# Optimization experiments

Hardware: AMD Instinct MI355X
Metric: run time of the kernel (lower is better)

Reference implementation:

```python
import jax, jax.numpy as jnp
import numpy as np
from jax import lax

SHIFT_SIZE = 5
PAD = SHIFT_SIZE // 2


def _shift(xn, axis):
    """xn: (B, C, Hp, Wp, Dp) zero-padded volume. Split channels into
    SHIFT_SIZE chunks and roll each chunk by shift in [-PAD, PAD] along `axis`."""
    chunks = jnp.split(xn, SHIFT_SIZE, axis=1)
    shifted = [jnp.roll(c, s, axis=axis) for c, s in zip(chunks, range(-PAD, PAD + 1))]
    return jnp.concatenate(shifted, axis=1)


def _shift_tokens(x, H, W, D, axis):
    """x: (B, N, C) tokens -> shifted tokens (B, N, C). axis=2 shifts H, axis=3 shifts W."""
    B, N, C = x.shape
    xn = x.transpose(0, 2, 1).reshape(B, C, H, W, D)
    xn = jnp.pad(xn, ((0, 0), (0, 0), (PAD, PAD), (PAD, PAD), (PAD, PAD)))
    xs = _shift(xn, axis)
    xs = xs[:, :, PAD:PAD + H, PAD:PAD + W, PAD:PAD + D]
    return xs.reshape(B, C, N).transpose(0, 2, 1)


def setup_inputs() -> dict:
    key = jax.random.key(0)
    ks = jax.random.split(key, 4)
    B, H, W, D = 2, 32, 32, 32
    N = H * W * D
    Cin, Ch = 160, 640
    return {
        "x": jax.random.normal(ks[0], (B, N, Cin), jnp.float32),
        "fc1_w": jax.random.normal(ks[1], (Ch, Cin), jnp.float32) * 0.02,
        "fc1_b": jnp.zeros((Ch,), jnp.float32),
        "dw_w": jax.random.normal(ks[2], (Ch, 1, 3, 3, 3), jnp.float32) * (2.0 / 27.0) ** 0.5,
        "dw_b": jnp.zeros((Ch,), jnp.float32),
        "fc2_w": jax.random.normal(ks[3], (Cin, Ch), jnp.float32) * 0.02,
        "fc2_b": jnp.zeros((Cin,), jnp.float32),
        "H": H, "W": W, "D": D,
    }


def reference(x, fc1_w, fc1_b, dw_w, dw_b, fc2_w, fc2_b, H, W, D):
    B, N, Cin = x.shape
    Ch = fc1_w.shape[0]
    # shift block 1: roll along H (axis 2)
    xs = _shift_tokens(x, H, W, D, axis=2)
    # fc1
    h = jnp.einsum('bnc,hc->bnh', xs, fc1_w) + fc1_b  # (B, N, Ch)
    # depthwise 3x3x3 conv
    hv = h.transpose(0, 2, 1).reshape(B, Ch, H, W, D)
    hv = lax.conv_general_dilated(
        hv, dw_w, window_strides=(1, 1, 1), padding='SAME',
        feature_group_count=Ch,
        dimension_numbers=('NCDHW', 'OIDHW', 'NCDHW'))
    hv = hv + dw_b[None, :, None, None, None]
    hv = jax.nn.gelu(hv, approximate=False)
    h = hv.reshape(B, Ch, N).transpose(0, 2, 1)
    # shift block 2: roll along W (axis 3)
    hs = _shift_tokens(h, H, W, D, axis=3)
    # fc2
    out = jnp.einsum('bnh,oh->bno', hs, fc2_w) + fc2_b  # (B, N, Cin)
    return out
```

## Files before the change

### kernel.cpp

```cpp
#include <hip/hip_runtime.h>
#include <hip/hip_bf16.h>
#include <math.h>

#define DEVI __device__ __forceinline__

typedef __bf16 bf16;
typedef _Float16 f16;
typedef bf16 bf16x4 __attribute__((ext_vector_type(4)));
typedef bf16 bf16x8 __attribute__((ext_vector_type(8)));
typedef f16 f16x8 __attribute__((ext_vector_type(8)));
typedef float f32x4 __attribute__((ext_vector_type(4)));

constexpr int Bb = 2, Hh = 32, Ww = 32, Dd = 32;
constexpr int Nn = Hh * Ww * Dd;
constexpr int BN = Bb * Nn;
constexpr int CIN = 160, CHH = 640;

constexpr size_t XB_OFF = 0;
constexpr size_t W1_OFF = XB_OFF + (size_t)BN * CIN * 2;
constexpr size_t W2_OFF = W1_OFF + (size_t)CHH * CIN * 2;
constexpr size_t WTH_OFF = W2_OFF + (size_t)CIN * CHH * 2;
constexpr size_t ZP_OFF = WTH_OFF + 34816;
constexpr size_t H1_OFF = ZP_OFF + 8192;
constexpr size_t H2_OFF = H1_OFF + (size_t)BN * CHH * 2;

DEVI void async16(const void* g, void* l) {
  __builtin_amdgcn_global_load_lds(
      (const __attribute__((address_space(1))) void*)g,
      (__attribute__((address_space(3))) void*)l, 16, 0, 0);
}

__global__ __launch_bounds__(256) void k_prep_x(const float* __restrict__ x,
                                                bf16* __restrict__ xb, int n4) {
  int i = blockIdx.x * 256 + threadIdx.x;
  if (i >= n4) return;
  float4 v = reinterpret_cast<const float4*>(x)[i];
  bf16x4 o;
  o[0] = (bf16)v.x; o[1] = (bf16)v.y; o[2] = (bf16)v.z; o[3] = (bf16)v.w;
  reinterpret_cast<bf16x4*>(xb)[i] = o;
}

__global__ __launch_bounds__(256) void k_prep_w(const float* __restrict__ fc1w,
                                                const float* __restrict__ fc2w,
                                                const float* __restrict__ dww,
                                                bf16* __restrict__ w1b,
                                                bf16* __restrict__ w2b,
                                                f16* __restrict__ wTh,
                                                unsigned* __restrict__ zp) {
  int i = blockIdx.x * 256 + threadIdx.x;
  const int NW = CHH * CIN;
  if (i < NW) {
    w1b[i] = (bf16)fc1w[i];
  } else if (i < 2 * NW) {
    int j = i - NW;
    w2b[j] = (bf16)fc2w[j];
  } else if (i < 2 * NW + 27 * CHH) {
    int j = i - 2 * NW;
    int ch = j / 27, tap = j % 27;
    wTh[tap * CHH + ch] = (f16)dww[j];
  } else if (i < 2 * NW + 27 * CHH + 2048) {
    zp[i - (2 * NW + 27 * CHH)] = 0u;
  }
}

__global__ __launch_bounds__(256) void k_gemm1(const bf16* __restrict__ xb,
                                               const bf16* __restrict__ w1b,
                                               const float* __restrict__ fc1b,
                                               const bf16* __restrict__ zp,
                                               f16* __restrict__ h1h) {
  __shared__ bf16 lsA[128 * 32];
  __shared__ bf16 lsB[128 * 32];
  const int tid = threadIdx.x;
  const int lane = tid & 63, wave = tid >> 6;
  const int row0 = blockIdx.x * 128;
  const int col0 = blockIdx.y * 128;

  f32x4 acc[4][4] = {};
  const int wr = wave >> 1, wc = wave & 1;
  const int rl = lane & 15, kb = (lane >> 4) * 8;

  for (int ks = 0; ks < 5; ++ks) {
    __syncthreads();
    const int s = ks - 2;
#pragma unroll
    for (int issue = 0; issue < 2; ++issue) {
      int c = issue * 256 + tid;
      int ar = c >> 2;
      int kc = (c & 3) * 8;
      int t = row0 + ar;
      int h = (t >> 10) & 31;
      int hs = h - s;
      const bf16* src;
      if (hs >= 0 && hs < 32)
        src = xb + (size_t)(t - s * 1024) * CIN + ks * 32 + kc;
      else
        src = zp + (size_t)(c & 63) * 8;
      async16(src, (char*)lsA + issue * 4096 + wave * 1024);
    }
#pragma unroll
    for (int issue = 0; issue < 2; ++issue) {
      int c = issue * 256 + tid;
      int br = c >> 2;
      int kc = (c & 3) * 8;
      const bf16* src = w1b + (size_t)(col0 + br) * CIN + ks * 32 + kc;
      async16(src, (char*)lsB + issue * 4096 + wave * 1024);
    }
    __syncthreads();
    bf16x8 af[4], bfr[4];
#pragma unroll
    for (int mi = 0; mi < 4; ++mi)
      af[mi] = *(const bf16x8*)&lsA[(wr * 64 + mi * 16 + rl) * 32 + kb];
#pragma unroll
    for (int ni = 0; ni < 4; ++ni)
      bfr[ni] = *(const bf16x8*)&lsB[(wc * 64 + ni * 16 + rl) * 32 + kb];
#pragma unroll
    for (int mi = 0; mi < 4; ++mi)
#pragma unroll
      for (int ni = 0; ni < 4; ++ni)
        acc[mi][ni] = __builtin_amdgcn_mfma_f32_16x16x32_bf16(af[mi], bfr[ni], acc[mi][ni], 0, 0, 0);
  }
  const int rq = lane >> 4;
#pragma unroll
  for (int mi = 0; mi < 4; ++mi) {
#pragma unroll
    for (int ni = 0; ni < 4; ++ni) {
      int col = col0 + wc * 64 + ni * 16 + rl;
      float bias = fc1b[col];
#pragma unroll
      for (int r = 0; r < 4; ++r) {
        int row = row0 + wr * 64 + mi * 16 + rq * 4 + r;
        h1h[(size_t)row * CHH + col] = (f16)(acc[mi][ni][r] + bias);
      }
    }
  }
}

__global__ __launch_bounds__(256) void k_conv(const f16* __restrict__ h1h,
                                              const f16* __restrict__ wTh,
                                              const float* __restrict__ dwb,
                                              const bf16* __restrict__ zp,
                                              bf16* __restrict__ h2b) {
  __shared__ f16 lw[27 * 64];
  __shared__ float lb[64];
  const int tid = threadIdx.x;
  const int cg = blockIdx.y;
#pragma unroll
  for (int i = 0; i < 7; ++i) {
    int idx = i * 256 + tid;
    if (idx < 27 * 64) lw[idx] = wTh[(idx >> 6) * CHH + cg * 64 + (idx & 63)];
  }
  if (tid < 64) lb[tid] = dwb[cg * 64 + tid];
  __syncthreads();

  const int lane = tid & 63, wave = tid >> 6;
  const int line = blockIdx.x * 4 + wave;
  const int c8 = lane & 7, dq = lane >> 3;
  const int d0 = dq * 4;
  const int ch0 = cg * 64 + c8 * 8;
  const int w = line & 31, h = (line >> 5) & 31;
  const f16* zpf = (const f16*)zp;

  f16x8 acc[4];
  {
    f16x8 binit;
#pragma unroll
    for (int j = 0; j < 8; ++j) binit[j] = (f16)lb[c8 * 8 + j];
    acc[0] = binit; acc[1] = binit; acc[2] = binit; acc[3] = binit;
  }

  const ptrdiff_t base_line = (ptrdiff_t)line * 32 * CHH + ch0;

#pragma unroll
  for (int kz = 0; kz < 3; ++kz) {
    int hz = h + kz - 1;
    if ((unsigned)hz >= 32u) continue;
#pragma unroll
    for (int ky = 0; ky < 3; ++ky) {
      int wy = w + ky - 1;
      if ((unsigned)wy >= 32u) continue;
      const f16* rowbase = h1h + base_line +
                           (ptrdiff_t)((kz - 1) * 1024 + (ky - 1) * 32) * CHH;
      f16x8 wt[3];
#pragma unroll
      for (int kx = 0; kx < 3; ++kx)
        wt[kx] = *(const f16x8*)&lw[((kz * 9 + ky * 3 + kx) << 6) + c8 * 8];
      f16x8 v[6];
#pragma unroll
      for (int j = 0; j < 6; ++j) {
        int td = d0 - 1 + j;
        const f16* p = ((unsigned)td < 32u) ? rowbase + (ptrdiff_t)td * CHH
                                            : zpf + c8 * 8;
        v[j] = *(const f16x8*)p;
      }
#pragma unroll
      for (int o = 0; o < 4; ++o)
#pragma unroll
        for (int kx = 0; kx < 3; ++kx)
          acc[o] = v[o + kx] * wt[kx] + acc[o];
    }
  }

#pragma unroll
  for (int o = 0; o < 4; ++o) {
    bf16x8 ovec;
#pragma unroll
    for (int j = 0; j < 8; ++j) {
      float xv = (float)acc[o][j];
      float zt = 0.7978845608f * xv + 0.03567740814f * (xv * xv * xv);
      zt = fminf(fmaxf(zt, -15.0f), 15.0f);
      float e = __builtin_exp2f(zt * 2.8853900817779268f);
      float tnh = (e - 1.0f) / (e + 1.0f);
      ovec[j] = (bf16)(0.5f * xv * (1.0f + tnh));
    }
    *(bf16x8*)&h2b[base_line + (ptrdiff_t)(d0 + o) * CHH] = ovec;
  }
}

__global__ __launch_bounds__(256) void k_gemm2(const bf16* __restrict__ h2b,
                                               const bf16* __restrict__ w2b,
                                               const float* __restrict__ fc2b,
                                               const bf16* __restrict__ zp,
                                               float* __restrict__ out) {
  __shared__ bf16 lsA[128 * 64];
  __shared__ bf16 lsB[160 * 64];
  const int tid = threadIdx.x, lane = tid & 63, wave = tid >> 6;
  const int row0 = blockIdx.x * 128;
  const int rl = lane & 15, kb = (lane >> 4) * 8;

  f32x4 acc[2][10] = {};

  for (int kt = 0; kt < 10; ++kt) {
    __syncthreads();
    const int k0 = kt * 64;
    const int s = (k0 >> 7) - 2;
#pragma unroll
    for (int issue = 0; issue < 4; ++issue) {
      int c = issue * 256 + tid;
      int ar = c >> 3;
      int kc = (c & 7) * 8;
      int t = row0 + ar;
      int w = (t >> 5) & 31;
      int wsv = w - s;
      const bf16* src;
      if (wsv >= 0 && wsv < 32)
        src = h2b + (size_t)(t - s * 32) * CHH + k0 + kc;
      else
        src = zp + (size_t)(c & 63) * 8;
      async16(src, (char*)lsA + issue * 4096 + wave * 1024);
    }
#pragma unroll
    for (int issue = 0; issue < 5; ++issue) {
      int c = issue * 256 + tid;
      int br = c >> 3;
      int kc = (c & 7) * 8;
      const bf16* src = w2b + (size_t)br * CHH + k0 + kc;
      async16(src, (char*)lsB + issue * 4096 + wave * 1024);
    }
    __syncthreads();
#pragma unroll
    for (int kk = 0; kk < 2; ++kk) {
      bf16x8 af[2], bfr[10];
#pragma unroll
      for (int mi = 0; mi < 2; ++mi)
        af[mi] = *(const bf16x8*)&lsA[(wave * 32 + mi * 16 + rl) * 64 + kk * 32 + kb];
#pragma unroll
      for (int ni = 0; ni < 10; ++ni)
        bfr[ni] = *(const bf16x8*)&lsB[(ni * 16 + rl) * 64 + kk * 32 + kb];
#pragma unroll
      for (int mi = 0; mi < 2; ++mi)
#pragma unroll
        for (int ni = 0; ni < 10; ++ni)
          acc[mi][ni] = __builtin_amdgcn_mfma_f32_16x16x32_bf16(af[mi], bfr[ni], acc[mi][ni], 0, 0, 0);
    }
  }
  const int rq = lane >> 4;
#pragma unroll
  for (int mi = 0; mi < 2; ++mi) {
#pragma unroll
    for (int ni = 0; ni < 10; ++ni) {
      int col = ni * 16 + rl;
      float bias = fc2b[col];
#pragma unroll
      for (int r = 0; r < 4; ++r) {
        int row = row0 + wave * 32 + mi * 16 + rq * 4 + r;
        out[(size_t)row * CIN + col] = acc[mi][ni][r] + bias;
      }
    }
  }
}

extern "C" void kernel_launch(void* const* d_in, const int* in_sizes, int n_in,
                              void* d_out, int out_size, void* d_ws, size_t ws_size,
                              hipStream_t stream) {
  const float* x    = (const float*)d_in[0];
  const float* fc1w = (const float*)d_in[1];
  const float* fc1b = (const float*)d_in[2];
  const float* dww  = (const float*)d_in[3];
  const float* dwb  = (const float*)d_in[4];
  const float* fc2w = (const float*)d_in[5];
  const float* fc2b = (const float*)d_in[6];

  char* ws = (char*)d_ws;
  bf16* xb   = (bf16*)(ws + XB_OFF);
  bf16* w1b  = (bf16*)(ws + W1_OFF);
  bf16* w2b  = (bf16*)(ws + W2_OFF);
  f16*  wTh  = (f16*)(ws + WTH_OFF);
  bf16* zp   = (bf16*)(ws + ZP_OFF);
  f16*  h1h  = (f16*)(ws + H1_OFF);
  bf16* h2b  = (bf16*)(ws + H2_OFF);
  float* out = (float*)d_out;

  k_prep_x<<<(BN * CIN / 4) / 256, 256, 0, stream>>>(x, xb, BN * CIN / 4);
  k_prep_w<<<943, 256, 0, stream>>>(fc1w, fc2w, dww, w1b, w2b, wTh, (unsigned*)zp);
  dim3 g1(512, 5);
  k_gemm1<<<g1, 256, 0, stream>>>(xb, w1b, fc1b, zp, h1h);
  dim3 gc(BN / 32 / 4, 10);
  k_conv<<<gc, 256, 0, stream>>>(h1h, wTh, dwb, zp, h2b);
  k_gemm2<<<512, 256, 0, stream>>>(h2b, w2b, fc2b, zp, out);
}
```

Measured before the change: 146.6 us.

## Store fc1 output into zero-padded volume to remove conv boundary checks

gemm1 now writes its output into a 34x34x34 zero-padded halo layout. A new kernel zeroes only the halo cells, so the depthwise conv loads all 27 taps without branching or selecting a zero-page pointer. The xb and h2b buffers now share one workspace region, and the GELU tanh form is rewritten as a sigmoid using exp2 and a hardware reciprocal. This adds an extra zeroing launch and a larger h1 buffer, and the sigmoid rewrite drops the clamp, so it relies on the reciprocal's behaviour at very large inputs.

```diff
diff --git a/kernel.cpp b/kernel.cpp
--- a/kernel.cpp
+++ b/kernel.cpp
@@ -15,14 +15,15 @@
 constexpr int Nn = Hh * Ww * Dd;
 constexpr int BN = Bb * Nn;
 constexpr int CIN = 160, CHH = 640;
-
-constexpr size_t XB_OFF = 0;
-constexpr size_t W1_OFF = XB_OFF + (size_t)BN * CIN * 2;
-constexpr size_t W2_OFF = W1_OFF + (size_t)CHH * CIN * 2;
+constexpr int PD = 34;
+constexpr int PT = PD * PD * PD;
+
+constexpr size_t W1_OFF  = 0;
+constexpr size_t W2_OFF  = W1_OFF + (size_t)CHH * CIN * 2;
 constexpr size_t WTH_OFF = W2_OFF + (size_t)CIN * CHH * 2;
-constexpr size_t ZP_OFF = WTH_OFF + 34816;
-constexpr size_t H1_OFF = ZP_OFF + 8192;
-constexpr size_t H2_OFF = H1_OFF + (size_t)BN * CHH * 2;
+constexpr size_t ZP_OFF  = WTH_OFF + 34816;
+constexpr size_t U_OFF   = 458752;
+constexpr size_t H1P_OFF = U_OFF + (size_t)BN * CHH * 2;
 
 DEVI void async16(const void* g, void* l) {
   __builtin_amdgcn_global_load_lds(
@@ -63,11 +64,27 @@
   }
 }
 
+__global__ __launch_bounds__(256) void k_zero_pad(f16* __restrict__ h1p) {
+  int g = blockIdx.x * 256 + threadIdx.x;
+  int p = g / 80;
+  int c = g - p * 80;
+  if (p >= 2 * PT) return;
+  int r = p % PT;
+  int hp = r / (PD * PD);
+  int r2 = r % (PD * PD);
+  int wp = r2 / PD, dp = r2 % PD;
+  bool pad = (hp == 0) | (hp == PD - 1) | (wp == 0) | (wp == PD - 1) |
+             (dp == 0) | (dp == PD - 1);
+  if (!pad) return;
+  f16x8 z = {};
+  *(f16x8*)&h1p[(size_t)p * CHH + c * 8] = z;
+}
+
 __global__ __launch_bounds__(256) void k_gemm1(const bf16* __restrict__ xb,
                                                const bf16* __restrict__ w1b,
                                                const float* __restrict__ fc1b,
                                                const bf16* __restrict__ zp,
-                                               f16* __restrict__ h1h) {
+                                               f16* __restrict__ h1p) {
   __shared__ bf16 lsA[128 * 32];
   __shared__ bf16 lsB[128 * 32];
   const int tid = threadIdx.x;
@@ -122,23 +139,26 @@
   const int rq = lane >> 4;
 #pragma unroll
   for (int mi = 0; mi < 4; ++mi) {
+    int rowq = row0 + wr * 64 + mi * 16 + rq * 4;
+    int bq = rowq >> 15;
+    int nq = rowq & 32767;
+    int hq = nq >> 10, wq = (nq >> 5) & 31, dq = nq & 31;
+    size_t pos = (size_t)((bq * PD + hq + 1) * PD + (wq + 1)) * PD + (dq + 1);
+    f16* dst0 = h1p + pos * CHH;
 #pragma unroll
     for (int ni = 0; ni < 4; ++ni) {
       int col = col0 + wc * 64 + ni * 16 + rl;
       float bias = fc1b[col];
 #pragma unroll
-      for (int r = 0; r < 4; ++r) {
-        int row = row0 + wr * 64 + mi * 16 + rq * 4 + r;
-        h1h[(size_t)row * CHH + col] = (f16)(acc[mi][ni][r] + bias);
-      }
-    }
-  }
-}
-
-__global__ __launch_bounds__(256) void k_conv(const f16* __restrict__ h1h,
+      for (int r = 0; r < 4; ++r)
+        dst0[(size_t)r * CHH + col] = (f16)(acc[mi][ni][r] + bias);
+    }
+  }
+}
+
+__global__ __launch_bounds__(256) void k_conv(const f16* __restrict__ h1p,
                                               const f16* __restrict__ wTh,
                                               const float* __restrict__ dwb,
-                                              const bf16* __restrict__ zp,
                                               bf16* __restrict__ h2b) {
   __shared__ f16 lw[27 * 64];
   __shared__ float lb[64];
@@ -157,8 +177,10 @@
   const int c8 = lane & 7, dq = lane >> 3;
   const int d0 = dq * 4;
   const int ch0 = cg * 64 + c8 * 8;
-  const int w = line & 31, h = (line >> 5) & 31;
-  const f16* zpf = (const f16*)zp;
+  const int w = line & 31, h = (line >> 5) & 31, b = line >> 10;
+
+  const size_t cidx = (size_t)((b * PD + h) * PD + w) * PD + d0;
+  const f16* base = h1p + cidx * CHH + ch0;
 
   f16x8 acc[4];
   {
@@ -168,30 +190,19 @@
     acc[0] = binit; acc[1] = binit; acc[2] = binit; acc[3] = binit;
   }
 
-  const ptrdiff_t base_line = (ptrdiff_t)line * 32 * CHH + ch0;
-
 #pragma unroll
   for (int kz = 0; kz < 3; ++kz) {
-    int hz = h + kz - 1;
-    if ((unsigned)hz >= 32u) continue;
 #pragma unroll
     for (int ky = 0; ky < 3; ++ky) {
-      int wy = w + ky - 1;
-      if ((unsigned)wy >= 32u) continue;
-      const f16* rowbase = h1h + base_line +
-                           (ptrdiff_t)((kz - 1) * 1024 + (ky - 1) * 32) * CHH;
+      const f16* pb = base + (size_t)(kz * PD + ky) * PD * CHH;
       f16x8 wt[3];
 #pragma unroll
       for (int kx = 0; kx < 3; ++kx)
         wt[kx] = *(const f16x8*)&lw[((kz * 9 + ky * 3 + kx) << 6) + c8 * 8];
       f16x8 v[6];
 #pragma unroll
-      for (int j = 0; j < 6; ++j) {
-        int td = d0 - 1 + j;
-        const f16* p = ((unsigned)td < 32u) ? rowbase + (ptrdiff_t)td * CHH
-                                            : zpf + c8 * 8;
-        v[j] = *(const f16x8*)p;
-      }
+      for (int j = 0; j < 6; ++j)
+        v[j] = *(const f16x8*)(pb + (size_t)j * CHH);
 #pragma unroll
       for (int o = 0; o < 4; ++o)
 #pragma unroll
@@ -200,19 +211,20 @@
     }
   }
 
+  const ptrdiff_t obase = (ptrdiff_t)(line * 32 + d0) * CHH + ch0;
 #pragma unroll
   for (int o = 0; o < 4; ++o) {
     bf16x8 ovec;
 #pragma unroll
     for (int j = 0; j < 8; ++j) {
       float xv = (float)acc[o][j];
-      float zt = 0.7978845608f * xv + 0.03567740814f * (xv * xv * xv);
-      zt = fminf(fmaxf(zt, -15.0f), 15.0f);
-      float e = __builtin_exp2f(zt * 2.8853900817779268f);
-      float tnh = (e - 1.0f) / (e + 1.0f);
-      ovec[j] = (bf16)(0.5f * xv * (1.0f + tnh));
-    }
-    *(bf16x8*)&h2b[base_line + (ptrdiff_t)(d0 + o) * CHH] = ovec;
+      float x2 = xv * xv;
+      float u = xv * (2.3022078f + 0.102943324f * x2);
+      float e = __builtin_exp2f(u);
+      float r = __builtin_amdgcn_rcpf(1.0f + e);
+      ovec[j] = (bf16)(xv - xv * r);
+    }
+    *(bf16x8*)&h2b[obase + (ptrdiff_t)o * CHH] = ovec;
   }
 }
 
@@ -301,20 +313,21 @@
   const float* fc2b = (const float*)d_in[6];
 
   char* ws = (char*)d_ws;
-  bf16* xb   = (bf16*)(ws + XB_OFF);
   bf16* w1b  = (bf16*)(ws + W1_OFF);
   bf16* w2b  = (bf16*)(ws + W2_OFF);
   f16*  wTh  = (f16*)(ws + WTH_OFF);
   bf16* zp   = (bf16*)(ws + ZP_OFF);
-  f16*  h1h  = (f16*)(ws + H1_OFF);
-  bf16* h2b  = (bf16*)(ws + H2_OFF);
+  bf16* xb   = (bf16*)(ws + U_OFF);
+  bf16* h2b  = (bf16*)(ws + U_OFF);
+  f16*  h1p  = (f16*)(ws + H1P_OFF);
   float* out = (float*)d_out;
 
+  k_zero_pad<<<(2 * PT * 80) / 256, 256, 0, stream>>>(h1p);
   k_prep_x<<<(BN * CIN / 4) / 256, 256, 0, stream>>>(x, xb, BN * CIN / 4);
   k_prep_w<<<943, 256, 0, stream>>>(fc1w, fc2w, dww, w1b, w2b, wTh, (unsigned*)zp);
   dim3 g1(512, 5);
-  k_gemm1<<<g1, 256, 0, stream>>>(xb, w1b, fc1b, zp, h1h);
+  k_gemm1<<<g1, 256, 0, stream>>>(xb, w1b, fc1b, zp, h1p);
   dim3 gc(BN / 32 / 4, 10);
-  k_conv<<<gc, 256, 0, stream>>>(h1h, wTh, dwb, zp, h2b);
+  k_conv<<<gc, 256, 0, stream>>>(h1p, wTh, dwb, h2b);
   k_gemm2<<<512, 256, 0, stream>>>(h2b, w2b, fc2b, zp, out);
 }
```

Result: no change. 146.0 us (-0.5%).
